# Kernel optimization log

Measured on AMD Instinct MI355X. Metric: run time of the kernel, lower is better.

The kernel has to match this reference:

```python
import jax, jax.numpy as jnp
import numpy as np

K = 20          # args.k
NEG = 0.2       # LeakyReLU negative slope

def lrelu(x):
    return jnp.where(x >= 0, x, NEG * x)

def bn(x, s, b):
    # eval-mode batchnorm folded into per-channel affine; channel axis = 1
    sh = (1, -1) + (1,) * (x.ndim - 2)
    return x * s.reshape(sh) + b.reshape(sh)

def se(x, w1, w2):
    # Squeeze-and-Excite on (B, C, N, k)
    y = jnp.mean(x, axis=(2, 3))                      # (B, C)
    y = jax.nn.sigmoid(jax.nn.relu(y @ w1.T) @ w2.T)  # (B, C)
    return x * y[:, :, None, None]

def graph_feature(x):
    # x: (B, C, N) -> edge features (B, 2C, N, K)
    xx = jnp.sum(x * x, axis=1)                        # (B, N)
    inner = jnp.einsum('bcn,bcm->bnm', x, x)           # (B, N, N)
    dist = -xx[:, :, None] + 2.0 * inner - xx[:, None, :]
    idx = jax.lax.top_k(dist, K)[1]                    # (B, N, K) nearest (incl. self)
    xt = jnp.transpose(x, (0, 2, 1))                   # (B, N, C)
    nbr = jax.vmap(lambda t, i: t[i])(xt, idx)         # (B, N, K, C)
    ctr = xt[:, :, None, :]
    out = jnp.concatenate([nbr - ctr, jnp.broadcast_to(ctr, nbr.shape)], axis=3)
    return jnp.transpose(out, (0, 3, 1, 2))

def edge_block(x, w, s, b, w1, w2):
    # get_graph_feature -> 1x1 conv -> BN -> SE -> LeakyReLU -> max over k
    g = graph_feature(x)                               # (B, 2C, N, K)
    h = jnp.einsum('bcnk,oc->bonk', g, w)
    h = lrelu(se(bn(h, s, b), w1, w2))
    return jnp.max(h, axis=-1)                         # (B, O, N)

def forward(x, conv1_w, conv2_w, conv3_w, conv4_w, conv5_w,
            bn1_s, bn1_b, bn2_s, bn2_b, bn3_s, bn3_b, bn4_s, bn4_b, bn5_s, bn5_b,
            se1_w1, se1_w2, se2_w1, se2_w2, se3_w1, se3_w2, se4_w1, se4_w2,
            res1_w, res2_w, res3_w,
            lin1_w, bn6_s, bn6_b, lin2_w, lin2_b, bn7_s, bn7_b, lin3_w, lin3_b):
    x1 = edge_block(x, conv1_w, bn1_s, bn1_b, se1_w1, se1_w2)                 # (B,512,N)
    x2 = edge_block(x1, conv2_w, bn2_s, bn2_b, se2_w1, se2_w2)
    x2 = x2 + jnp.einsum('bcn,oc->bon', x1, res1_w)                           # (B,512,N)
    x3 = edge_block(x2, conv3_w, bn3_s, bn3_b, se3_w1, se3_w2)
    x3 = x3 + jnp.einsum('bcn,oc->bon', x2, res2_w)                           # (B,1024,N)
    x4 = edge_block(x3, conv4_w, bn4_s, bn4_b, se4_w1, se4_w2)
    x4 = x4 + jnp.einsum('bcn,oc->bon', x3, res3_w)                           # (B,1024,N)
    h = jnp.concatenate([x1, x2, x3, x4], axis=1)                             # (B,3072,N)
    h = lrelu(bn(jnp.einsum('bcn,oc->bon', h, conv5_w), bn5_s, bn5_b))        # (B,2048,N)
    f = jnp.concatenate([jnp.max(h, axis=-1), jnp.mean(h, axis=-1)], axis=1)  # (B,4096)
    f = lrelu(bn(f @ lin1_w.T, bn6_s, bn6_b))       # dropout is eval-mode identity
    f = lrelu(bn(f @ lin2_w.T + lin2_b, bn7_s, bn7_b))
    return f @ lin3_w.T + lin3_b                    # (B,40)

def setup_inputs():
    ks = jax.random.split(jax.random.key(0), 40)
    B, N = 16, 128
    f32 = jnp.float32
    def w(i, shape, s=0.02):
        return jax.random.normal(ks[i], shape, f32) * s
    def bns(i, c):
        return 1.0 + 0.1 * jax.random.normal(ks[i], (c,), f32)
    def bnb(i, c):
        return 0.1 * jax.random.normal(ks[i], (c,), f32)
    return {
        'x': jax.random.normal(ks[0], (B, 512, N), f32),
        'conv1_w': w(1, (512, 1024)),
        'conv2_w': w(2, (512, 1024)),
        'conv3_w': w(3, (1024, 1024)),
        'conv4_w': w(4, (1024, 2048)),
        'conv5_w': w(5, (2048, 3072)),
        'bn1_s': bns(6, 512), 'bn1_b': bnb(7, 512),
        'bn2_s': bns(8, 512), 'bn2_b': bnb(9, 512),
        'bn3_s': bns(10, 1024), 'bn3_b': bnb(11, 1024),
        'bn4_s': bns(12, 1024), 'bn4_b': bnb(13, 1024),
        'bn5_s': bns(14, 2048), 'bn5_b': bnb(15, 2048),
        'se1_w1': w(16, (32, 512), 0.05), 'se1_w2': w(17, (512, 32), 0.05),
        'se2_w1': w(18, (32, 512), 0.05), 'se2_w2': w(19, (512, 32), 0.05),
        'se3_w1': w(20, (64, 1024), 0.05), 'se3_w2': w(21, (1024, 64), 0.05),
        'se4_w1': w(22, (64, 1024), 0.05), 'se4_w2': w(23, (1024, 64), 0.05),
        'res1_w': w(24, (512, 512)),
        'res2_w': w(25, (1024, 512)),
        'res3_w': w(26, (1024, 1024)),
        'lin1_w': w(27, (512, 4096)),
        'bn6_s': bns(28, 512), 'bn6_b': bnb(29, 512),
        'lin2_w': w(30, (256, 512)), 'lin2_b': bnb(31, 256),
        'bn7_s': bns(32, 256), 'bn7_b': bnb(33, 256),
        'lin3_w': w(34, (40, 256)), 'lin3_b': bnb(35, 40),
    }

def reference(x, conv1_w, conv2_w, conv3_w, conv4_w, conv5_w,
              bn1_s, bn1_b, bn2_s, bn2_b, bn3_s, bn3_b, bn4_s, bn4_b, bn5_s, bn5_b,
              se1_w1, se1_w2, se2_w1, se2_w2, se3_w1, se3_w2, se4_w1, se4_w2,
              res1_w, res2_w, res3_w,
              lin1_w, bn6_s, bn6_b, lin2_w, lin2_b, bn7_s, bn7_b, lin3_w, lin3_b):
    return forward(x, conv1_w, conv2_w, conv3_w, conv4_w, conv5_w,
                   bn1_s, bn1_b, bn2_s, bn2_b, bn3_s, bn3_b, bn4_s, bn4_b, bn5_s, bn5_b,
                   se1_w1, se1_w2, se2_w1, se2_w2, se3_w1, se3_w2, se4_w1, se4_w2,
                   res1_w, res2_w, res3_w,
                   lin1_w, bn6_s, bn6_b, lin2_w, lin2_b, bn7_s, bn7_b, lin3_w, lin3_b)
```

## Files before the change

### kernel.cpp

```cpp
#include <hip/hip_runtime.h>
#include <hip/hip_bf16.h>


#define BN_ALL 2048
typedef __hip_bfloat16 bf16;
typedef __attribute__((ext_vector_type(8))) short short8;
typedef __attribute__((ext_vector_type(4))) float float4v;

__device__ __forceinline__ float b2f(bf16 v) { return __bfloat162float(v); }
__device__ __forceinline__ float lrelu(float v) { return v >= 0.f ? v : 0.2f * v; }
__device__ __forceinline__ short f2bs(float v) {
    bf16 h = __float2bfloat16(v);
    return *reinterpret_cast<short*>(&h);
}

__device__ __forceinline__ void gll16(const void* g, void* l) {
    __builtin_amdgcn_global_load_lds(
        (const __attribute__((address_space(1))) unsigned int*)g,
        (__attribute__((address_space(3))) unsigned int*)l,
        16, 0, 0);
}

__device__ __forceinline__ float ldin(const void* p, size_t i, int isb) {
    return isb ? __bfloat162float(((const bf16*)p)[i]) : ((const float*)p)[i];
}

__device__ __forceinline__ float ld1(const float* p) { return *p; }
__device__ __forceinline__ float ld1(const bf16* p)  { return __bfloat162float(*p); }
__device__ __forceinline__ void st1(float* p, float v) { *p = v; }
__device__ __forceinline__ void st1(bf16* p, float v)  { *p = __float2bfloat16(v); }
__device__ __forceinline__ short ldbs(const float* p) { return f2bs(*p); }
__device__ __forceinline__ short ldbs(const bf16* p)  { return *(const short*)p; }

__global__ __launch_bounds__(256) void detect_dtype(const void* __restrict__ x, int* __restrict__ flag) {
    const unsigned* u = (const unsigned*)x;
    int sane = 0;
    for (int i = threadIdx.x; i < 4096; i += 256) {
        unsigned e = (u[i] >> 23) & 0xFF;
        sane += (e >= 87 && e <= 167) ? 1 : 0;
    }
    __shared__ int sh[256];
    sh[threadIdx.x] = sane;
    __syncthreads();
    for (int off = 128; off > 0; off >>= 1) {
        if (threadIdx.x < off) sh[threadIdx.x] += sh[threadIdx.x + off];
        __syncthreads();
    }
    if (threadIdx.x == 0) *flag = (sh[0] < 2048) ? 1 : 0;
}

__global__ __launch_bounds__(256) void convert_kp(const void* __restrict__ x, bf16* __restrict__ X0,
                                                  const int* __restrict__ dflag) {
    int isb = *dflag;
    int item = blockIdx.x * 256 + threadIdx.x;
    int cg = item >> 11, bn = item & 2047;
    int b = bn >> 7, n = bn & 127;
    short8 pk;
#pragma unroll
    for (int j = 0; j < 8; ++j)
        pk[j] = f2bs(ldin(x, ((size_t)(b * 512 + cg * 8 + j)) * 128 + n, isb));
    *(short8*)((short*)X0 + ((size_t)cg * BN_ALL + bn) * 8) = pk;
}

__global__ __launch_bounds__(256) void gram_k(const bf16* __restrict__ X, int C,
                                              float* __restrict__ G) {
    __shared__ __align__(16) short Bsm[2][8192];
    int tid = threadIdx.x;
    int b = blockIdx.x;
    int lane = tid & 63, wv = tid >> 6, wm = wv & 1, wn = wv >> 1;
    int lq = lane >> 4, lr = lane & 15;
    int KC = C >> 6;
    const short* Xs = (const short*)X;

    float4v acc[4][4];
#pragma unroll
    for (int i = 0; i < 4; i++)
#pragma unroll
        for (int j = 0; j < 4; j++) acc[i][j] = (float4v){0.f, 0.f, 0.f, 0.f};

#pragma unroll
    for (int it = 0; it < 4; ++it) {
        int i = tid + it * 256;
        int q = i >> 7, c = i & 127;
        gll16(Xs + ((size_t)q * BN_ALL + b * 128 + c) * 8, &Bsm[0][(size_t)i * 8]);
    }
    __syncthreads();

    int p = 0;
    for (int kc = 0; kc < KC; ++kc) {
        if (kc + 1 < KC) {
#pragma unroll
            for (int it = 0; it < 4; ++it) {
                int i = tid + it * 256;
                int q = i >> 7, c = i & 127;
                gll16(Xs + ((size_t)((kc + 1) * 8 + q) * BN_ALL + b * 128 + c) * 8,
                      &Bsm[p ^ 1][(size_t)i * 8]);
            }
        }
#pragma unroll
        for (int h = 0; h < 2; ++h) {
            short8 av[4], bv[4];
#pragma unroll
            for (int mt = 0; mt < 4; ++mt)
                av[mt] = *(const short8*)&Bsm[p][(size_t)(h * 512 + (lq << 7) + wm * 64 + mt * 16 + lr) * 8];
#pragma unroll
            for (int nt = 0; nt < 4; ++nt)
                bv[nt] = *(const short8*)&Bsm[p][(size_t)(h * 512 + (lq << 7) + wn * 64 + nt * 16 + lr) * 8];
#pragma unroll
            for (int mt = 0; mt < 4; ++mt)
#pragma unroll
                for (int nt = 0; nt < 4; ++nt)
                    acc[mt][nt] = __builtin_amdgcn_mfma_f32_16x16x32_bf16(av[mt], bv[nt], acc[mt][nt], 0, 0, 0);
        }
        __syncthreads();
        p ^= 1;
    }

    float* Gb = G + (size_t)b * 16384;
#pragma unroll
    for (int mt = 0; mt < 4; ++mt)
#pragma unroll
        for (int r = 0; r < 4; ++r) {
            int row = wm * 64 + mt * 16 + lq * 4 + r;
#pragma unroll
            for (int nt = 0; nt < 4; ++nt) {
                int col = wn * 64 + nt * 16 + lr;
                Gb[row * 128 + col] = acc[mt][nt][r];
            }
        }
}

__global__ __launch_bounds__(256) void topk_k(const float* __restrict__ G, int* __restrict__ idx) {
    int gw = (blockIdx.x * 256 + threadIdx.x) >> 6;
    int lane = threadIdx.x & 63;
    int b = gw >> 7, n = gw & 127;
    const float* Gb = G + (size_t)b * 16384;
    float g0 = Gb[n * 128 + lane];
    float g1 = Gb[n * 128 + 64 + lane];
    float dnn = Gb[n * 129];
    float dm0 = Gb[lane * 129];
    float dm1 = Gb[(64 + lane) * 129];
    float d0 = 2.f * g0 - dnn - dm0;
    float d1 = 2.f * g1 - dnn - dm1;
#pragma unroll
    for (int k = 0; k < 20; ++k) {
        float v; int i;
        if (d1 > d0) { v = d1; i = 64 + lane; } else { v = d0; i = lane; }
#pragma unroll
        for (int off = 1; off < 64; off <<= 1) {
            float ov = __shfl_xor(v, off, 64);
            int   oi = __shfl_xor(i, off, 64);
            if (ov > v || (ov == v && oi < i)) { v = ov; i = oi; }
        }
        if (lane == 0) idx[gw * 20 + k] = i;
        if (i < 64) { if (lane == i) d0 = -3.0e38f; }
        else        { if (lane == i - 64) d1 = -3.0e38f; }
    }
}

template <typename S>
__global__ __launch_bounds__(128) void knn_topk(const S* __restrict__ X, int C, int* __restrict__ idx) {
    int b = blockIdx.x >> 7;
    int n = blockIdx.x & 127;
    int m = threadIdx.x;
    const S* base = X + b * 128;
    float s0 = 0, s1 = 0, q0 = 0, q1 = 0;
    for (int c = 0; c < C; c += 2) {
        const S* p = base + (size_t)c * BN_ALL;
        float xm0 = ld1(p + m),          xn0 = ld1(p + n);
        float xm1 = ld1(p + BN_ALL + m), xn1 = ld1(p + BN_ALL + n);
        s0 += xm0 * xn0; q0 += xm0 * xm0;
        s1 += xm1 * xn1; q1 += xm1 * xm1;
    }
    float inner = s0 + s1;
    float xxm   = q0 + q1;
    __shared__ float xx[128];
    __shared__ float dist[128];
    __shared__ float rv[128];
    __shared__ int   ri[128];
    xx[m] = xxm;
    __syncthreads();
    dist[m] = 2.0f * inner - xx[n] - xxm;
    for (int k = 0; k < 20; k++) {
        __syncthreads();
        rv[m] = dist[m]; ri[m] = m;
        __syncthreads();
        for (int off = 64; off > 0; off >>= 1) {
            if (m < off) {
                float a = rv[m], bv = rv[m + off];
                int ia = ri[m], ib = ri[m + off];
                if (bv > a || (bv == a && ib < ia)) { rv[m] = bv; ri[m] = ib; }
            }
            __syncthreads();
        }
        if (m == 0) { idx[blockIdx.x * 20 + k] = ri[0]; dist[ri[0]] = -3.0e38f; }
    }
}

__global__ __launch_bounds__(256) void pack_w(const void* __restrict__ w, int ldw,
                                              const void* __restrict__ res, int Cin, int O,
                                              int Mtot, int K, short* __restrict__ out,
                                              const int* __restrict__ dflag) {
    int isb = *dflag;
    int item = blockIdx.x * 256 + threadIdx.x;
    if (item >= Mtot * (K >> 3)) return;
    int m_local = item & 127;
    int rest = item >> 7;
    int q = rest & 3; rest >>= 2;
    int KC = K >> 5;
    int kc = rest % KC, tm = rest / KC;
    int grow = tm * 128 + m_local;
    int k = kc * 32 + q * 8;
    const void* src; size_t base; int dif = 0;
    if (grow < O)          { src = w;   base = (size_t)grow * ldw + k; }
    else if (grow < 2 * O) { src = w;   base = (size_t)(grow - O) * ldw + k; dif = 1; }
    else                   { src = res; base = (size_t)(grow - 2 * O) * Cin + k; }
    short8 pk;
#pragma unroll
    for (int j = 0; j < 8; ++j) {
        float v = ldin(src, base + j, isb);
        if (dif) v = ldin(src, base + Cin + j, isb) - v;
        pk[j] = f2bs(v);
    }
    *(short8*)&out[(size_t)item * 8] = pk;
}

__global__ __launch_bounds__(256) void gemm_pk(const short* __restrict__ packA,
                                               const bf16* __restrict__ X, float* __restrict__ Cm, int K,
                                               const void* __restrict__ bnS, const void* __restrict__ bnB,
                                               int act, const int* __restrict__ dflag) {
    __shared__ __align__(16) short Asm[2][8192];
    __shared__ __align__(16) short Bsm[2][4096];
    int tid = threadIdx.x;
    int bm  = blockIdx.x << 7;
    int bn0 = blockIdx.y << 6;
    int lane = tid & 63, wv = tid >> 6, wm = wv & 1, wn = wv >> 1;
    int lq = lane >> 4, lr = lane & 15;
    int KC = K >> 6;
    const short* abase = packA + (size_t)blockIdx.x * (K >> 5) * 4096;
    const short* Xs = (const short*)X;
    int bq = tid >> 6, bc = tid & 63;

    float4v acc[4][2];
#pragma unroll
    for (int i = 0; i < 4; i++)
#pragma unroll
        for (int j = 0; j < 2; j++) acc[i][j] = (float4v){0.f, 0.f, 0.f, 0.f};

#pragma unroll
    for (int it = 0; it < 4; ++it)
        gll16(abase + (size_t)(tid + it * 256) * 8, &Asm[0][(size_t)(tid + it * 256) * 8]);
    gll16(Xs + ((size_t)bq * BN_ALL + bn0 + bc) * 8,       &Bsm[0][(size_t)tid * 8]);
    gll16(Xs + ((size_t)(bq + 4) * BN_ALL + bn0 + bc) * 8, &Bsm[0][(size_t)(tid + 256) * 8]);
    __syncthreads();

    int p = 0;
    for (int kc = 0; kc < KC; ++kc) {
        if (kc + 1 < KC) {
            const short* ab = abase + (size_t)(kc + 1) * 8192;
#pragma unroll
            for (int it = 0; it < 4; ++it)
                gll16(ab + (size_t)(tid + it * 256) * 8, &Asm[p ^ 1][(size_t)(tid + it * 256) * 8]);
            gll16(Xs + ((size_t)((kc + 1) * 8 + bq) * BN_ALL + bn0 + bc) * 8,
                  &Bsm[p ^ 1][(size_t)tid * 8]);
            gll16(Xs + ((size_t)((kc + 1) * 8 + bq + 4) * BN_ALL + bn0 + bc) * 8,
                  &Bsm[p ^ 1][(size_t)(tid + 256) * 8]);
        }
#pragma unroll
        for (int h = 0; h < 2; ++h) {
            short8 av[4], bv[2];
#pragma unroll
            for (int mt = 0; mt < 4; ++mt)
                av[mt] = *(const short8*)&Asm[p][(size_t)(h * 512 + (lq << 7) + wm * 64 + mt * 16 + lr) * 8];
#pragma unroll
            for (int nt = 0; nt < 2; ++nt)
                bv[nt] = *(const short8*)&Bsm[p][(size_t)(h * 256 + (lq << 6) + wn * 32 + nt * 16 + lr) * 8];
#pragma unroll
            for (int mt = 0; mt < 4; ++mt)
#pragma unroll
                for (int nt = 0; nt < 2; ++nt)
                    acc[mt][nt] = __builtin_amdgcn_mfma_f32_16x16x32_bf16(av[mt], bv[nt], acc[mt][nt], 0, 0, 0);
        }
        __syncthreads();
        p ^= 1;
    }

    int isb = *dflag;
#pragma unroll
    for (int mt = 0; mt < 4; ++mt) {
#pragma unroll
        for (int r = 0; r < 4; ++r) {
            int row = bm + wm * 64 + mt * 16 + lq * 4 + r;
            float s = 1.f, bb = 0.f;
            if (bnS) { s = ldin(bnS, row, isb); bb = ldin(bnB, row, isb); }
#pragma unroll
            for (int nt = 0; nt < 2; ++nt) {
                int col = bn0 + wn * 32 + nt * 16 + lr;
                float v = acc[mt][nt][r];
                if (bnS) v = v * s + bb;
                if (act) v = lrelu(v);
                Cm[(size_t)row * BN_ALL + col] = v;
            }
        }
    }
}

template <typename S>
__global__ __launch_bounds__(256) void gemm_mfma(const void* __restrict__ w, int ldw,
                                                 const void* __restrict__ res, int Cin, int O,
                                                 const S* __restrict__ X, S* __restrict__ Cm, int K,
                                                 const void* __restrict__ bnS, const void* __restrict__ bnB,
                                                 int act, const int* __restrict__ dflag) {
    int isb = *dflag;
    __shared__ short Asm[4096];
    __shared__ short Bsm[4096];
    int tid = threadIdx.x;
    int bm  = blockIdx.x << 7;
    int bn0 = blockIdx.y << 7;
    int lane = tid & 63, wv = tid >> 6;
    int wm = wv & 1, wn = wv >> 1;
    int lq = lane >> 4, lr = lane & 15;

    float4v acc[4][4];
#pragma unroll
    for (int i = 0; i < 4; i++)
#pragma unroll
        for (int j = 0; j < 4; j++) acc[i][j] = (float4v){0.f, 0.f, 0.f, 0.f};

    for (int k0 = 0; k0 < K; k0 += 32) {
#pragma unroll
        for (int it = 0; it < 2; ++it) {
            int i = tid + it * 256;
            int m = i >> 2, q = i & 3;
            int grow = bm + m;
            const void* asrc; size_t abase; int dif = 0;
            if (grow < O)          { asrc = w;   abase = (size_t)grow * ldw; }
            else if (grow < 2 * O) { asrc = w;   abase = (size_t)(grow - O) * ldw; dif = 1; }
            else                   { asrc = res; abase = (size_t)(grow - 2 * O) * Cin; }
            size_t kk = (size_t)k0 + q * 8;
            short8 pk;
#pragma unroll
            for (int j = 0; j < 8; ++j) {
                float v = ldin(asrc, abase + kk + j, isb);
                if (dif) v = ldin(asrc, abase + Cin + kk + j, isb) - v;
                pk[j] = f2bs(v);
            }
            *(short8*)&Asm[(size_t)(q * 128 + m) * 8] = pk;
        }
#pragma unroll
        for (int it = 0; it < 2; ++it) {
            int i = tid + it * 256;
            int q = i >> 7, c = i & 127;
            const S* xp = X + (size_t)(k0 + q * 8) * BN_ALL + bn0 + c;
            short8 pk;
#pragma unroll
            for (int j = 0; j < 8; ++j) pk[j] = f2bs(ld1(xp + (size_t)j * BN_ALL));
            *(short8*)&Bsm[(size_t)i * 8] = pk;
        }
        __syncthreads();
        short8 av[4], bv[4];
#pragma unroll
        for (int mt = 0; mt < 4; ++mt)
            av[mt] = *(const short8*)&Asm[(size_t)((lq << 7) + wm * 64 + mt * 16 + lr) * 8];
#pragma unroll
        for (int nt = 0; nt < 4; ++nt)
            bv[nt] = *(const short8*)&Bsm[(size_t)((lq << 7) + wn * 64 + nt * 16 + lr) * 8];
#pragma unroll
        for (int mt = 0; mt < 4; ++mt)
#pragma unroll
            for (int nt = 0; nt < 4; ++nt)
                acc[mt][nt] = __builtin_amdgcn_mfma_f32_16x16x32_bf16(av[mt], bv[nt], acc[mt][nt], 0, 0, 0);
        __syncthreads();
    }
#pragma unroll
    for (int mt = 0; mt < 4; ++mt) {
#pragma unroll
        for (int r = 0; r < 4; ++r) {
            int row = bm + wm * 64 + mt * 16 + lq * 4 + r;
            float s = 1.f, bb = 0.f;
            if (bnS) { s = ldin(bnS, row, isb); bb = ldin(bnB, row, isb); }
#pragma unroll
            for (int nt = 0; nt < 4; ++nt) {
                int col = bn0 + wn * 64 + nt * 16 + lr;
                float v = acc[mt][nt][r];
                if (bnS) v = v * s + bb;
                if (act) v = lrelu(v);
                st1(Cm + (size_t)row * BN_ALL + col, v);
            }
        }
    }
}

template <typename S>
__global__ __launch_bounds__(128) void gather_pool(S* __restrict__ PS, const int* __restrict__ idx,
                                                   const void* __restrict__ bns, const void* __restrict__ bnb,
                                                   float* __restrict__ Mb, int O,
                                                   const int* __restrict__ dflag) {
    int isb = *dflag;
    int o = blockIdx.x, b = blockIdx.y, n = threadIdx.x;
    S* Prow = PS + (size_t)o * BN_ALL + b * 128;
    const int* id = idx + (b * 128 + n) * 20;
    float mx = -3.0e38f, mn = 3.0e38f, sm = 0.f;
#pragma unroll
    for (int k = 0; k < 20; k++) {
        float p = ld1(Prow + id[k]);
        mx = fmaxf(mx, p); mn = fminf(mn, p); sm += p;
    }
    float Sv = ld1(PS + (size_t)(O + o) * BN_ALL + b * 128 + n);
    __shared__ float r1[128], r2[128];
    r1[n] = sm; r2[n] = Sv;
    __syncthreads();
    float s = ldin(bns, o, isb), bb = ldin(bnb, o, isb);
    float ext = (s >= 0.f) ? mx : mn;
    st1(Prow + n, lrelu(s * (ext + Sv) + bb));
    for (int off = 64; off > 0; off >>= 1) {
        if (n < off) { r1[n] += r1[n + off]; r2[n] += r2[n + off]; }
        __syncthreads();
    }
    if (n == 0) Mb[b * O + o] = s * (r1[0] * (1.f / 2560.f) + r2[0] * (1.f / 128.f)) + bb;
}

__global__ __launch_bounds__(256) void se1_k(const float* __restrict__ Mb, const void* __restrict__ w1,
                                             float* __restrict__ Z, int O, int r,
                                             const int* __restrict__ dflag) {
    int isb = *dflag;
    int gw = (blockIdx.x * 256 + threadIdx.x) >> 6;
    int lane = threadIdx.x & 63;
    int b = gw / r, t = gw - b * r;
    const float* mv = Mb + (size_t)b * O;
    float acc = 0.f;
    for (int c = lane; c < O; c += 64) acc += ldin(w1, (size_t)t * O + c, isb) * mv[c];
#pragma unroll
    for (int off = 32; off > 0; off >>= 1) acc += __shfl_xor(acc, off, 64);
    if (lane == 0) Z[b * r + t] = fmaxf(acc, 0.f);
}

__global__ __launch_bounds__(256) void se2_k(const float* __restrict__ Z, const void* __restrict__ w2,
                                             float* __restrict__ Y, int O, int r,
                                             const int* __restrict__ dflag) {
    int isb = *dflag;
    int gw = (blockIdx.x * 256 + threadIdx.x) >> 6;
    int lane = threadIdx.x & 63;
    int b = gw / O, o = gw - b * O;
    float acc = 0.f;
    if (lane < r) acc = ldin(w2, (size_t)o * r + lane, isb) * Z[b * r + lane];
#pragma unroll
    for (int off = 32; off > 0; off >>= 1) acc += __shfl_xor(acc, off, 64);
    if (lane == 0) Y[b * O + o] = 1.f / (1.f + expf(-acc));
}

__global__ __launch_bounds__(256) void se_k(const float* __restrict__ Mb, const void* __restrict__ w1,
                                            const void* __restrict__ w2, float* __restrict__ Y, int O, int r,
                                            const int* __restrict__ dflag) {
    int isb = *dflag;
    int b = blockIdx.x, t = threadIdx.x;
    __shared__ float mloc[1024];
    __shared__ float z[64];
    for (int i = t; i < O; i += 256) mloc[i] = Mb[b * O + i];
    __syncthreads();
    if (t < r) {
        float acc = 0.f;
        for (int c = 0; c < O; c++) acc += ldin(w1, (size_t)t * O + c, isb) * mloc[c];
        z[t] = fmaxf(acc, 0.f);
    }
    __syncthreads();
    for (int o = t; o < O; o += 256) {
        float acc = 0.f;
        for (int j = 0; j < r; j++) acc += ldin(w2, (size_t)o * r + j, isb) * z[j];
        Y[b * O + o] = 1.f / (1.f + expf(-acc));
    }
}

__global__ __launch_bounds__(256) void finalize_kp(const float* __restrict__ PS, const float* __restrict__ Y,
                                                   int useR, bf16* __restrict__ Xdst, int O) {
    int item = blockIdx.x * 256 + threadIdx.x;
    int og = item >> 11, bn = item & 2047;
    int b = bn >> 7;
    short8 pk;
#pragma unroll
    for (int j = 0; j < 8; ++j) {
        int r = og * 8 + j;
        float v = Y[b * O + r] * PS[(size_t)r * BN_ALL + bn];
        if (useR) v += PS[(size_t)(2 * O + r) * BN_ALL + bn];
        pk[j] = f2bs(v);
    }
    *(short8*)((short*)Xdst + ((size_t)og * BN_ALL + bn) * 8) = pk;
}

template <typename SP, typename SD>
__global__ __launch_bounds__(256) void finalize(const SP* __restrict__ PS, const float* __restrict__ Y,
                                                int useR, SD* __restrict__ Xdst, int O) {
    int tid = blockIdx.x * 256 + threadIdx.x;
    int o = tid >> 11, bn = tid & 2047;
    int b = bn >> 7;
    float v = Y[b * O + o] * ld1(PS + tid);
    if (useR) v += ld1(PS + (size_t)(2 * O + o) * BN_ALL + bn);
    st1(Xdst + tid, v);
}

template <typename S>
__global__ __launch_bounds__(256) void convert_x(const void* __restrict__ x, S* __restrict__ X0,
                                                 const int* __restrict__ dflag) {
    int isb = *dflag;
    int tid = blockIdx.x * 256 + threadIdx.x;
    int c = tid >> 11, bn = tid & 2047;
    int b = bn >> 7, n = bn & 127;
    st1(X0 + tid, ldin(x, (size_t)(b * 512 + c) * 128 + n, isb));
}

template <typename S>
__global__ __launch_bounds__(128) void pool5(const S* __restrict__ H, float* __restrict__ f) {
    int m = blockIdx.x, b = blockIdx.y, n = threadIdx.x;
    float v = ld1(H + (size_t)m * BN_ALL + b * 128 + n);
    __shared__ float rmx[128], rsm[128];
    rmx[n] = v; rsm[n] = v;
    __syncthreads();
    for (int off = 64; off > 0; off >>= 1) {
        if (n < off) { rmx[n] = fmaxf(rmx[n], rmx[n + off]); rsm[n] += rsm[n + off]; }
        __syncthreads();
    }
    if (n == 0) {
        f[b * 4096 + m] = rmx[0];
        f[b * 4096 + 2048 + m] = rsm[0] * (1.f / 128.f);
    }
}

__global__ __launch_bounds__(256) void head_k(const float* __restrict__ in, const void* __restrict__ W,
                                              const void* __restrict__ bias, const void* __restrict__ bns,
                                              const void* __restrict__ bnb, float* __restrict__ outf,
                                              void* __restrict__ outb, int Kd, int Od, int act,
                                              const int* __restrict__ dflag) {
    int isb = *dflag;
    int gw = (blockIdx.x * 256 + threadIdx.x) >> 6;
    int lane = threadIdx.x & 63;
    if (gw >= 16 * Od) return;
    int b = gw / Od, o = gw - b * Od;
    const float* iv = in + b * Kd;
    float acc = 0.f;
    for (int k = lane; k < Kd; k += 64) acc += iv[k] * ldin(W, (size_t)o * Kd + k, isb);
    for (int off = 32; off > 0; off >>= 1) acc += __shfl_xor(acc, off, 64);
    if (lane == 0) {
        float v = acc;
        if (bias) v += ldin(bias, o, isb);
        if (bns) v = v * ldin(bns, o, isb) + ldin(bnb, o, isb);
        if (act) v = lrelu(v);
        if (outb) {
            if (isb) ((bf16*)outb)[gw] = __float2bfloat16(v);
            else     ((float*)outb)[gw] = v;
        } else outf[gw] = v;
    }
}

__global__ __launch_bounds__(256) void zero_out(bf16* o, int n) {
    int i = blockIdx.x * 256 + threadIdx.x;
    if (i < n) o[i] = __float2bfloat16(0.f);
}

#define UNPACK_INPUTS()                                                     \
    const void* x_in   = d_in[0];                                           \
    const void* conv1w = d_in[1];  const void* conv2w = d_in[2];            \
    const void* conv3w = d_in[3];  const void* conv4w = d_in[4];            \
    const void* conv5w = d_in[5];                                           \
    const void* bn1s = d_in[6],  * bn1b = d_in[7];                          \
    const void* bn2s = d_in[8],  * bn2b = d_in[9];                          \
    const void* bn3s = d_in[10], * bn3b = d_in[11];                         \
    const void* bn4s = d_in[12], * bn4b = d_in[13];                         \
    const void* bn5s = d_in[14], * bn5b = d_in[15];                         \
    const void* se1w1 = d_in[16], * se1w2 = d_in[17];                       \
    const void* se2w1 = d_in[18], * se2w2 = d_in[19];                       \
    const void* se3w1 = d_in[20], * se3w2 = d_in[21];                       \
    const void* se4w1 = d_in[22], * se4w2 = d_in[23];                       \
    const void* res1w = d_in[24]; const void* res2w = d_in[25];             \
    const void* res3w = d_in[26]; const void* lin1w = d_in[27];             \
    const void* bn6s = d_in[28], * bn6b = d_in[29];                         \
    const void* lin2w = d_in[30], * lin2b = d_in[31];                       \
    const void* bn7s = d_in[32], * bn7b = d_in[33];                         \
    const void* lin3w = d_in[34], * lin3b = d_in[35];

static void run_net_packed(void* const* d_in, void* d_out, void* d_ws, hipStream_t stream) {
    UNPACK_INPUTS();
    float* WS = (float*)d_ws;
    float* PS   = WS;
    bf16*  XC   = (bf16*)(WS + 6291456);
    short* PACK = (short*)(WS + 12582912);
    float* MB = WS + 15728640;
    float* YB = MB + 16384;
    float* FB = YB + 16384;
    float* F1 = FB + 65536;
    float* F2 = F1 + 8192;
    int* IDX  = (int*)(F2 + 4096);
    int* DFLAG = IDX + 40960;
    float* ZB = (float*)(DFLAG + 16);
    bf16*  X0 = (bf16*)(PS + (size_t)2048 * BN_ALL);
    float* GRAM = PS;
    bf16* X1 = XC;
    bf16* X2 = XC + (size_t)512 * BN_ALL;
    bf16* X3 = XC + (size_t)1024 * BN_ALL;
    bf16* X4 = XC + (size_t)2048 * BN_ALL;

    detect_dtype<<<1, 256, 0, stream>>>(x_in, DFLAG);
    convert_kp<<<512, 256, 0, stream>>>(x_in, X0, DFLAG);

    gram_k<<<16, 256, 0, stream>>>(X0, 512, GRAM);
    topk_k<<<512, 256, 0, stream>>>(GRAM, IDX);
    pack_w<<<256, 256, 0, stream>>>(conv1w, 1024, nullptr, 512, 512, 1024, 512, PACK, DFLAG);
    gemm_pk<<<dim3(8, 32), 256, 0, stream>>>(PACK, X0, PS, 512, nullptr, nullptr, 0, DFLAG);
    gather_pool<float><<<dim3(512, 16), 128, 0, stream>>>(PS, IDX, bn1s, bn1b, MB, 512, DFLAG);
    se1_k<<<128, 256, 0, stream>>>(MB, se1w1, ZB, 512, 32, DFLAG);
    se2_k<<<2048, 256, 0, stream>>>(ZB, se1w2, YB, 512, 32, DFLAG);
    finalize_kp<<<512, 256, 0, stream>>>(PS, YB, 0, X1, 512);

    gram_k<<<16, 256, 0, stream>>>(X1, 512, GRAM);
    topk_k<<<512, 256, 0, stream>>>(GRAM, IDX);
    pack_w<<<384, 256, 0, stream>>>(conv2w, 1024, res1w, 512, 512, 1536, 512, PACK, DFLAG);
    gemm_pk<<<dim3(12, 32), 256, 0, stream>>>(PACK, X1, PS, 512, nullptr, nullptr, 0, DFLAG);
    gather_pool<float><<<dim3(512, 16), 128, 0, stream>>>(PS, IDX, bn2s, bn2b, MB, 512, DFLAG);
    se1_k<<<128, 256, 0, stream>>>(MB, se2w1, ZB, 512, 32, DFLAG);
    se2_k<<<2048, 256, 0, stream>>>(ZB, se2w2, YB, 512, 32, DFLAG);
    finalize_kp<<<512, 256, 0, stream>>>(PS, YB, 1, X2, 512);

    gram_k<<<16, 256, 0, stream>>>(X2, 512, GRAM);
    topk_k<<<512, 256, 0, stream>>>(GRAM, IDX);
    pack_w<<<768, 256, 0, stream>>>(conv3w, 1024, res2w, 512, 1024, 3072, 512, PACK, DFLAG);
    gemm_pk<<<dim3(24, 32), 256, 0, stream>>>(PACK, X2, PS, 512, nullptr, nullptr, 0, DFLAG);
    gather_pool<float><<<dim3(1024, 16), 128, 0, stream>>>(PS, IDX, bn3s, bn3b, MB, 1024, DFLAG);
    se1_k<<<256, 256, 0, stream>>>(MB, se3w1, ZB, 1024, 64, DFLAG);
    se2_k<<<4096, 256, 0, stream>>>(ZB, se3w2, YB, 1024, 64, DFLAG);
    finalize_kp<<<1024, 256, 0, stream>>>(PS, YB, 1, X3, 1024);

    gram_k<<<16, 256, 0, stream>>>(X3, 1024, GRAM);
    topk_k<<<512, 256, 0, stream>>>(GRAM, IDX);
    pack_w<<<1536, 256, 0, stream>>>(conv4w, 2048, res3w, 1024, 1024, 3072, 1024, PACK, DFLAG);
    gemm_pk<<<dim3(24, 32), 256, 0, stream>>>(PACK, X3, PS, 1024, nullptr, nullptr, 0, DFLAG);
    gather_pool<float><<<dim3(1024, 16), 128, 0, stream>>>(PS, IDX, bn4s, bn4b, MB, 1024, DFLAG);
    se1_k<<<256, 256, 0, stream>>>(MB, se4w1, ZB, 1024, 64, DFLAG);
    se2_k<<<4096, 256, 0, stream>>>(ZB, se4w2, YB, 1024, 64, DFLAG);
    finalize_kp<<<1024, 256, 0, stream>>>(PS, YB, 1, X4, 1024);

    pack_w<<<3072, 256, 0, stream>>>(conv5w, 3072, nullptr, 3072, 2048, 2048, 3072, PACK, DFLAG);
    gemm_pk<<<dim3(16, 32), 256, 0, stream>>>(PACK, XC, PS, 3072, bn5s, bn5b, 1, DFLAG);
    pool5<float><<<dim3(2048, 16), 128, 0, stream>>>(PS, FB);

    head_k<<<2048, 256, 0, stream>>>(FB, lin1w, nullptr, bn6s, bn6b, F1, nullptr, 4096, 512, 1, DFLAG);
    head_k<<<1024, 256, 0, stream>>>(F1, lin2w, lin2b, bn7s, bn7b, F2, nullptr, 512, 256, 1, DFLAG);
    head_k<<<160, 256, 0, stream>>>(F2, lin3w, lin3b, nullptr, nullptr, nullptr, d_out, 256, 40, 0, DFLAG);
}

template <typename S>
static void run_net(void* const* d_in, void* d_out, void* d_ws, hipStream_t stream) {
    UNPACK_INPUTS();
    const size_t RC = (size_t)3072 * BN_ALL;
    S* PS = (S*)d_ws;
    S* XC = PS + RC;
    S* X0 = PS + (size_t)2048 * BN_ALL;
    float* MB = (float*)(XC + RC);
    float* YB = MB + 16 * 1024;
    float* FB = YB + 16 * 1024;
    float* F1 = FB + 16 * 4096;
    float* F2 = F1 + 16 * 512;
    int* IDX  = (int*)(F2 + 16 * 256);
    int* DFLAG = IDX + 16 * 128 * 20;

    S* X1 = XC;
    S* X2 = XC + (size_t)512 * BN_ALL;
    S* X3 = XC + (size_t)1024 * BN_ALL;
    S* X4 = XC + (size_t)2048 * BN_ALL;

    detect_dtype<<<1, 256, 0, stream>>>(x_in, DFLAG);
    convert_x<S><<<4096, 256, 0, stream>>>(x_in, X0, DFLAG);

    knn_topk<S><<<2048, 128, 0, stream>>>(X0, 512, IDX);
    gemm_mfma<S><<<dim3(8, 16), 256, 0, stream>>>(conv1w, 1024, nullptr, 512, 512, X0, PS, 512, nullptr, nullptr, 0, DFLAG);
    gather_pool<S><<<dim3(512, 16), 128, 0, stream>>>(PS, IDX, bn1s, bn1b, MB, 512, DFLAG);
    se_k<<<16, 256, 0, stream>>>(MB, se1w1, se1w2, YB, 512, 32, DFLAG);
    finalize<S, S><<<4096, 256, 0, stream>>>(PS, YB, 0, X1, 512);

    knn_topk<S><<<2048, 128, 0, stream>>>(X1, 512, IDX);
    gemm_mfma<S><<<dim3(12, 16), 256, 0, stream>>>(conv2w, 1024, res1w, 512, 512, X1, PS, 512, nullptr, nullptr, 0, DFLAG);
    gather_pool<S><<<dim3(512, 16), 128, 0, stream>>>(PS, IDX, bn2s, bn2b, MB, 512, DFLAG);
    se_k<<<16, 256, 0, stream>>>(MB, se2w1, se2w2, YB, 512, 32, DFLAG);
    finalize<S, S><<<4096, 256, 0, stream>>>(PS, YB, 1, X2, 512);

    knn_topk<S><<<2048, 128, 0, stream>>>(X2, 512, IDX);
    gemm_mfma<S><<<dim3(24, 16), 256, 0, stream>>>(conv3w, 1024, res2w, 512, 1024, X2, PS, 512, nullptr, nullptr, 0, DFLAG);
    gather_pool<S><<<dim3(1024, 16), 128, 0, stream>>>(PS, IDX, bn3s, bn3b, MB, 1024, DFLAG);
    se_k<<<16, 256, 0, stream>>>(MB, se3w1, se3w2, YB, 1024, 64, DFLAG);
    finalize<S, S><<<8192, 256, 0, stream>>>(PS, YB, 1, X3, 1024);

    knn_topk<S><<<2048, 128, 0, stream>>>(X3, 1024, IDX);
    gemm_mfma<S><<<dim3(24, 16), 256, 0, stream>>>(conv4w, 2048, res3w, 1024, 1024, X3, PS, 1024, nullptr, nullptr, 0, DFLAG);
    gather_pool<S><<<dim3(1024, 16), 128, 0, stream>>>(PS, IDX, bn4s, bn4b, MB, 1024, DFLAG);
    se_k<<<16, 256, 0, stream>>>(MB, se4w1, se4w2, YB, 1024, 64, DFLAG);
    finalize<S, S><<<8192, 256, 0, stream>>>(PS, YB, 1, X4, 1024);

    gemm_mfma<S><<<dim3(16, 16), 256, 0, stream>>>(conv5w, 3072, nullptr, 3072, 2048, XC, PS, 3072, bn5s, bn5b, 1, DFLAG);
    pool5<S><<<dim3(2048, 16), 128, 0, stream>>>(PS, FB);

    head_k<<<2048, 256, 0, stream>>>(FB, lin1w, nullptr, bn6s, bn6b, F1, nullptr, 4096, 512, 1, DFLAG);
    head_k<<<1024, 256, 0, stream>>>(F1, lin2w, lin2b, bn7s, bn7b, F2, nullptr, 512, 256, 1, DFLAG);
    head_k<<<160, 256, 0, stream>>>(F2, lin3w, lin3b, nullptr, nullptr, nullptr, d_out, 256, 40, 0, DFLAG);
}

extern "C" void kernel_launch(void* const* d_in, const int* in_sizes, int n_in,
                              void* d_out, int out_size, void* d_ws, size_t ws_size,
                              hipStream_t stream) {
    const size_t SMALL = (16 * 1024 + 16 * 1024 + 16 * 4096 + 16 * 512 + 16 * 256) * 4
                       + 16 * 128 * 20 * 4 + 8192;
    const size_t NEED_PACKED = (size_t)15728640 * 4 + SMALL;
    const size_t NEED_F32    = 2 * ((size_t)3072 * BN_ALL * 4) + SMALL;
    const size_t NEED_BF16   = 2 * ((size_t)3072 * BN_ALL * 2) + SMALL;
    if (ws_size >= NEED_PACKED) {
        run_net_packed(d_in, d_out, d_ws, stream);
    } else if (ws_size >= NEED_F32) {
        run_net<float>(d_in, d_out, d_ws, stream);
    } else if (ws_size >= NEED_BF16) {
        run_net<bf16>(d_in, d_out, d_ws, stream);
    } else {
        zero_out<<<3, 256, 0, stream>>>((bf16*)d_out, out_size);
    }
}
```

Measured before the change: 599.1 us.

## Triple-buffer LDS in gram and packed GEMM kernels with partial vmcnt waits

Changes the gram and packed GEMM kernels from double to triple buffering of global-to-LDS loads, prefetching two K-chunks ahead. The full __syncthreads drain is replaced by explicit partial s_waitcnt vmcnt counts and raw s_barrier, so the loads for later chunks stay in flight while the current chunk is computed. This hides more global-load latency at the cost of 50% more LDS per block, which may reduce occupancy. It also relies on hand-counted vmcnt values matching the number of issued loads.

```diff
diff --git a/kernel.cpp b/kernel.cpp
--- a/kernel.cpp
+++ b/kernel.cpp
@@ -64,7 +64,7 @@
 
 __global__ __launch_bounds__(256) void gram_k(const bf16* __restrict__ X, int C,
                                               float* __restrict__ G) {
-    __shared__ __align__(16) short Bsm[2][8192];
+    __shared__ __align__(16) short Bsm[3][8192];
     int tid = threadIdx.x;
     int b = blockIdx.x;
     int lane = tid & 63, wv = tid >> 6, wm = wv & 1, wn = wv >> 1;
@@ -79,41 +79,49 @@
         for (int j = 0; j < 4; j++) acc[i][j] = (float4v){0.f, 0.f, 0.f, 0.f};
 
 #pragma unroll
-    for (int it = 0; it < 4; ++it) {
-        int i = tid + it * 256;
-        int q = i >> 7, c = i & 127;
-        gll16(Xs + ((size_t)q * BN_ALL + b * 128 + c) * 8, &Bsm[0][(size_t)i * 8]);
-    }
-    __syncthreads();
-
-    int p = 0;
+    for (int t = 0; t < 2; ++t)
+#pragma unroll
+        for (int it = 0; it < 4; ++it) {
+            int i = tid + it * 256;
+            int q = i >> 7, c = i & 127;
+            gll16(Xs + ((size_t)(t * 8 + q) * BN_ALL + b * 128 + c) * 8,
+                  &Bsm[t][(size_t)i * 8]);
+        }
+
     for (int kc = 0; kc < KC; ++kc) {
-        if (kc + 1 < KC) {
+        if (kc + 2 < KC) {
+            int tb = (kc + 2) % 3;
 #pragma unroll
             for (int it = 0; it < 4; ++it) {
                 int i = tid + it * 256;
                 int q = i >> 7, c = i & 127;
-                gll16(Xs + ((size_t)((kc + 1) * 8 + q) * BN_ALL + b * 128 + c) * 8,
-                      &Bsm[p ^ 1][(size_t)i * 8]);
+                gll16(Xs + ((size_t)((kc + 2) * 8 + q) * BN_ALL + b * 128 + c) * 8,
+                      &Bsm[tb][(size_t)i * 8]);
             }
         }
+        if (kc + 2 < KC)      asm volatile("s_waitcnt vmcnt(8)" ::: "memory");
+        else if (kc + 1 < KC) asm volatile("s_waitcnt vmcnt(4)" ::: "memory");
+        else                  asm volatile("s_waitcnt vmcnt(0)" ::: "memory");
+        __builtin_amdgcn_s_barrier();
+        __builtin_amdgcn_sched_barrier(0);
+        const short* bp = &Bsm[kc % 3][0];
 #pragma unroll
         for (int h = 0; h < 2; ++h) {
             short8 av[4], bv[4];
 #pragma unroll
             for (int mt = 0; mt < 4; ++mt)
-                av[mt] = *(const short8*)&Bsm[p][(size_t)(h * 512 + (lq << 7) + wm * 64 + mt * 16 + lr) * 8];
+                av[mt] = *(const short8*)&bp[(size_t)(h * 512 + (lq << 7) + wm * 64 + mt * 16 + lr) * 8];
 #pragma unroll
             for (int nt = 0; nt < 4; ++nt)
-                bv[nt] = *(const short8*)&Bsm[p][(size_t)(h * 512 + (lq << 7) + wn * 64 + nt * 16 + lr) * 8];
+                bv[nt] = *(const short8*)&bp[(size_t)(h * 512 + (lq << 7) + wn * 64 + nt * 16 + lr) * 8];
 #pragma unroll
             for (int mt = 0; mt < 4; ++mt)
 #pragma unroll
                 for (int nt = 0; nt < 4; ++nt)
                     acc[mt][nt] = __builtin_amdgcn_mfma_f32_16x16x32_bf16(av[mt], bv[nt], acc[mt][nt], 0, 0, 0);
         }
-        __syncthreads();
-        p ^= 1;
+        __builtin_amdgcn_sched_barrier(0);
+        __builtin_amdgcn_s_barrier();
     }
 
     float* Gb = G + (size_t)b * 16384;
@@ -229,8 +237,8 @@
                                                const bf16* __restrict__ X, float* __restrict__ Cm, int K,
                                                const void* __restrict__ bnS, const void* __restrict__ bnB,
                                                int act, const int* __restrict__ dflag) {
-    __shared__ __align__(16) short Asm[2][8192];
-    __shared__ __align__(16) short Bsm[2][4096];
+    __shared__ __align__(16) short Asm[3][8192];
+    __shared__ __align__(16) short Bsm[3][4096];
     int tid = threadIdx.x;
     int bm  = blockIdx.x << 7;
     int bn0 = blockIdx.y << 6;
@@ -248,41 +256,52 @@
         for (int j = 0; j < 2; j++) acc[i][j] = (float4v){0.f, 0.f, 0.f, 0.f};
 
 #pragma unroll
-    for (int it = 0; it < 4; ++it)
-        gll16(abase + (size_t)(tid + it * 256) * 8, &Asm[0][(size_t)(tid + it * 256) * 8]);
-    gll16(Xs + ((size_t)bq * BN_ALL + bn0 + bc) * 8,       &Bsm[0][(size_t)tid * 8]);
-    gll16(Xs + ((size_t)(bq + 4) * BN_ALL + bn0 + bc) * 8, &Bsm[0][(size_t)(tid + 256) * 8]);
-    __syncthreads();
-
-    int p = 0;
+    for (int t = 0; t < 2; ++t) {
+        const short* ab = abase + (size_t)t * 8192;
+#pragma unroll
+        for (int it = 0; it < 4; ++it)
+            gll16(ab + (size_t)(tid + it * 256) * 8, &Asm[t][(size_t)(tid + it * 256) * 8]);
+        gll16(Xs + ((size_t)(t * 8 + bq) * BN_ALL + bn0 + bc) * 8,       &Bsm[t][(size_t)tid * 8]);
+        gll16(Xs + ((size_t)(t * 8 + bq + 4) * BN_ALL + bn0 + bc) * 8,   &Bsm[t][(size_t)(tid + 256) * 8]);
+    }
+
     for (int kc = 0; kc < KC; ++kc) {
-        if (kc + 1 < KC) {
-            const short* ab = abase + (size_t)(kc + 1) * 8192;
+        if (kc + 2 < KC) {
+            int tb = (kc + 2) % 3;
+            const short* ab = abase + (size_t)(kc + 2) * 8192;
 #pragma unroll
             for (int it = 0; it < 4; ++it)
-                gll16(ab + (size_t)(tid + it * 256) * 8, &Asm[p ^ 1][(size_t)(tid + it * 256) * 8]);
-            gll16(Xs + ((size_t)((kc + 1) * 8 + bq) * BN_ALL + bn0 + bc) * 8,
-                  &Bsm[p ^ 1][(size_t)tid * 8]);
-            gll16(Xs + ((size_t)((kc + 1) * 8 + bq + 4) * BN_ALL + bn0 + bc) * 8,
-                  &Bsm[p ^ 1][(size_t)(tid + 256) * 8]);
-        }
+                gll16(ab + (size_t)(tid + it * 256) * 8, &Asm[tb][(size_t)(tid + it * 256) * 8]);
+            gll16(Xs + ((size_t)((kc + 2) * 8 + bq) * BN_ALL + bn0 + bc) * 8,
+                  &Bsm[tb][(size_t)tid * 8]);
+            gll16(Xs + ((size_t)((kc + 2) * 8 + bq + 4) * BN_ALL + bn0 + bc) * 8,
+                  &Bsm[tb][(size_t)(tid + 256) * 8]);
+        }
+        if (kc + 2 < KC)      asm volatile("s_waitcnt vmcnt(12)" ::: "memory");
+        else if (kc + 1 < KC) asm volatile("s_waitcnt vmcnt(6)" ::: "memory");
+        else                  asm volatile("s_waitcnt vmcnt(0)" ::: "memory");
+        __builtin_amdgcn_s_barrier();
+        __builtin_amdgcn_sched_barrier(0);
+        int p = kc % 3;
+        const short* ap = &Asm[p][0];
+        const short* bp = &Bsm[p][0];
 #pragma unroll
         for (int h = 0; h < 2; ++h) {
             short8 av[4], bv[2];
 #pragma unroll
             for (int mt = 0; mt < 4; ++mt)
-                av[mt] = *(const short8*)&Asm[p][(size_t)(h * 512 + (lq << 7) + wm * 64 + mt * 16 + lr) * 8];
+                av[mt] = *(const short8*)&ap[(size_t)(h * 512 + (lq << 7) + wm * 64 + mt * 16 + lr) * 8];
 #pragma unroll
             for (int nt = 0; nt < 2; ++nt)
-                bv[nt] = *(const short8*)&Bsm[p][(size_t)(h * 256 + (lq << 6) + wn * 32 + nt * 16 + lr) * 8];
+                bv[nt] = *(const short8*)&bp[(size_t)(h * 256 + (lq << 6) + wn * 32 + nt * 16 + lr) * 8];
 #pragma unroll
             for (int mt = 0; mt < 4; ++mt)
 #pragma unroll
                 for (int nt = 0; nt < 2; ++nt)
                     acc[mt][nt] = __builtin_amdgcn_mfma_f32_16x16x32_bf16(av[mt], bv[nt], acc[mt][nt], 0, 0, 0);
         }
-        __syncthreads();
-        p ^= 1;
+        __builtin_amdgcn_sched_barrier(0);
+        __builtin_amdgcn_s_barrier();
     }
 
     int isb = *dflag;
```

New measurement: 642.3 us. 1.07x slower.

## Load packed A operand directly into registers, bypassing LDS, in gemm_pk

Applied to the files above, without the earlier changes.

The packed weight (A) tiles are now read straight from global memory into registers with a two-stage register double buffer (arA/arB), and the A shared-memory buffers are removed. The main loop is unrolled by two so each half uses a fixed LDS buffer for B. This cuts LDS traffic and shared-memory footprint, which may allow more occupancy. It adds register pressure, and the loop assumes KC is even.

```diff
diff --git a/kernel.cpp b/kernel.cpp
--- a/kernel.cpp
+++ b/kernel.cpp
@@ -229,7 +229,6 @@
                                                const bf16* __restrict__ X, float* __restrict__ Cm, int K,
                                                const void* __restrict__ bnS, const void* __restrict__ bnB,
                                                int act, const int* __restrict__ dflag) {
-    __shared__ __align__(16) short Asm[2][8192];
     __shared__ __align__(16) short Bsm[2][4096];
     int tid = threadIdx.x;
     int bm  = blockIdx.x << 7;
@@ -240,6 +239,7 @@
     const short* abase = packA + (size_t)blockIdx.x * (K >> 5) * 4096;
     const short* Xs = (const short*)X;
     int bq = tid >> 6, bc = tid & 63;
+    int aoff = (lq * 128 + wm * 64 + lr) * 8;
 
     float4v acc[4][2];
 #pragma unroll
@@ -247,42 +247,69 @@
 #pragma unroll
         for (int j = 0; j < 2; j++) acc[i][j] = (float4v){0.f, 0.f, 0.f, 0.f};
 
-#pragma unroll
-    for (int it = 0; it < 4; ++it)
-        gll16(abase + (size_t)(tid + it * 256) * 8, &Asm[0][(size_t)(tid + it * 256) * 8]);
+    short8 arA[8], arB[8];
+
     gll16(Xs + ((size_t)bq * BN_ALL + bn0 + bc) * 8,       &Bsm[0][(size_t)tid * 8]);
     gll16(Xs + ((size_t)(bq + 4) * BN_ALL + bn0 + bc) * 8, &Bsm[0][(size_t)(tid + 256) * 8]);
+#pragma unroll
+    for (int h = 0; h < 2; ++h)
+#pragma unroll
+        for (int mt = 0; mt < 4; ++mt)
+            arA[h * 4 + mt] = *(const short8*)&abase[(size_t)h * 4096 + aoff + mt * 128];
     __syncthreads();
 
-    int p = 0;
-    for (int kc = 0; kc < KC; ++kc) {
-        if (kc + 1 < KC) {
+    for (int kc = 0; kc < KC; kc += 2) {
+        {
             const short* ab = abase + (size_t)(kc + 1) * 8192;
-#pragma unroll
-            for (int it = 0; it < 4; ++it)
-                gll16(ab + (size_t)(tid + it * 256) * 8, &Asm[p ^ 1][(size_t)(tid + it * 256) * 8]);
             gll16(Xs + ((size_t)((kc + 1) * 8 + bq) * BN_ALL + bn0 + bc) * 8,
-                  &Bsm[p ^ 1][(size_t)tid * 8]);
+                  &Bsm[1][(size_t)tid * 8]);
             gll16(Xs + ((size_t)((kc + 1) * 8 + bq + 4) * BN_ALL + bn0 + bc) * 8,
-                  &Bsm[p ^ 1][(size_t)(tid + 256) * 8]);
+                  &Bsm[1][(size_t)(tid + 256) * 8]);
+#pragma unroll
+            for (int h = 0; h < 2; ++h)
+#pragma unroll
+                for (int mt = 0; mt < 4; ++mt)
+                    arB[h * 4 + mt] = *(const short8*)&ab[(size_t)h * 4096 + aoff + mt * 128];
         }
 #pragma unroll
         for (int h = 0; h < 2; ++h) {
-            short8 av[4], bv[2];
+            short8 bv[2];
+#pragma unroll
+            for (int nt = 0; nt < 2; ++nt)
+                bv[nt] = *(const short8*)&Bsm[0][(size_t)(h * 256 + (lq << 6) + wn * 32 + nt * 16 + lr) * 8];
 #pragma unroll
             for (int mt = 0; mt < 4; ++mt)
-                av[mt] = *(const short8*)&Asm[p][(size_t)(h * 512 + (lq << 7) + wm * 64 + mt * 16 + lr) * 8];
+#pragma unroll
+                for (int nt = 0; nt < 2; ++nt)
+                    acc[mt][nt] = __builtin_amdgcn_mfma_f32_16x16x32_bf16(arA[h * 4 + mt], bv[nt], acc[mt][nt], 0, 0, 0);
+        }
+        __syncthreads();
+
+        if (kc + 2 < KC) {
+            const short* ab = abase + (size_t)(kc + 2) * 8192;
+            gll16(Xs + ((size_t)((kc + 2) * 8 + bq) * BN_ALL + bn0 + bc) * 8,
+                  &Bsm[0][(size_t)tid * 8]);
+            gll16(Xs + ((size_t)((kc + 2) * 8 + bq + 4) * BN_ALL + bn0 + bc) * 8,
+                  &Bsm[0][(size_t)(tid + 256) * 8]);
+#pragma unroll
+            for (int h = 0; h < 2; ++h)
+#pragma unroll
+                for (int mt = 0; mt < 4; ++mt)
+                    arA[h * 4 + mt] = *(const short8*)&ab[(size_t)h * 4096 + aoff + mt * 128];
+        }
+#pragma unroll
+        for (int h = 0; h < 2; ++h) {
+            short8 bv[2];
 #pragma unroll
             for (int nt = 0; nt < 2; ++nt)
-                bv[nt] = *(const short8*)&Bsm[p][(size_t)(h * 256 + (lq << 6) + wn * 32 + nt * 16 + lr) * 8];
+                bv[nt] = *(const short8*)&Bsm[1][(size_t)(h * 256 + (lq << 6) + wn * 32 + nt * 16 + lr) * 8];
 #pragma unroll
             for (int mt = 0; mt < 4; ++mt)
 #pragma unroll
                 for (int nt = 0; nt < 2; ++nt)
-                    acc[mt][nt] = __builtin_amdgcn_mfma_f32_16x16x32_bf16(av[mt], bv[nt], acc[mt][nt], 0, 0, 0);
-        }
-        __syncthreads();
-        p ^= 1;
+                    acc[mt][nt] = __builtin_amdgcn_mfma_f32_16x16x32_bf16(arB[h * 4 + mt], bv[nt], acc[mt][nt], 0, 0, 0);
+        }
+        __syncthreads();
     }
 
     int isb = *dflag;
```

Result: slower. 632.9 us (+5.6%).
